# Optimization experiments

Hardware: AMD Instinct MI355X
Metric: run time of the kernel (lower is better)

Reference implementation:

```python
import jax, jax.numpy as jnp
import numpy as np

BS, TS, NE, ED = 32, 64, 64, 96
E = 256        # attn_embed_dim
H = 4          # attn_n_heads
HD = E // H    # head dim
RNN_H = 256
N_ACT = 32
NA = 16        # n_agents


def setup_inputs():
    key = jax.random.key(0)
    ks = jax.random.split(key, 40)
    entities = jax.random.normal(ks[0], (BS, TS, NE, ED), jnp.float32)
    obs_mask = jax.random.randint(ks[1], (BS, TS, NE, NE), 0, 2).astype(jnp.float32)  # 1 = masked
    entity_mask = (jax.random.uniform(ks[2], (BS, TS, NE)) < 0.1).astype(jnp.float32)  # 1 = inactive
    hidden_state = jnp.zeros((BS * NA, RNN_H), jnp.float32)
    it = iter(range(3, 40))
    def lin(fi, fo):
        return jax.random.normal(ks[next(it)], (fi, fo), jnp.float32) / np.sqrt(fi).astype(np.float32)
    p = dict(
        fc1_w=lin(ED, E), fc1_b=jnp.zeros((E,), jnp.float32),
        attn_in_w=lin(E, 3 * E), attn_out_w=lin(E, E), attn_out_b=jnp.zeros((E,), jnp.float32),
        fc2_w=lin(2 * E, RNN_H), fc2_b=jnp.zeros((RNN_H,), jnp.float32),
        gru_w_ih=lin(RNN_H, 3 * RNN_H), gru_w_hh=lin(RNN_H, 3 * RNN_H),
        gru_b_ih=jnp.zeros((3 * RNN_H,), jnp.float32), gru_b_hh=jnp.zeros((3 * RNN_H,), jnp.float32),
        fc3_w=lin(RNN_H, N_ACT), fc3_b=jnp.zeros((N_ACT,), jnp.float32),
        fcmsg1_w=lin(ED, E), fcmsg1_b=jnp.zeros((E,), jnp.float32),
        lmsg_in_w=lin(E, 3 * E), lmsg_out_w=lin(E, E), lmsg_out_b=jnp.zeros((E,), jnp.float32),
        gmsg_in_w=lin(E, 3 * E), gmsg_out_w=lin(E, E), gmsg_out_b=jnp.zeros((E,), jnp.float32),
        gate_in_w=lin(E, 3 * E), gate_out_w=lin(E, E), gate_out_b=jnp.zeros((E,), jnp.float32),
        gatefc1_w=lin(ED, E), gatefc1_b=jnp.zeros((E,), jnp.float32),
        gatefc2_w=lin(E, 2), gatefc2_b=jnp.zeros((2,), jnp.float32),
    )
    return dict(entities=entities, obs_mask=obs_mask, entity_mask=entity_mask,
                hidden_state=hidden_state, **p)


def _attn(x, in_w, out_w, out_b, pre_mask, post_mask):
    """REFIL EntityAttentionLayer: n_queries = NA agent rows, masks use 1 = masked."""
    B, ne, e = x.shape
    q, k, v = jnp.split(x @ in_w, 3, axis=-1)                       # each [B, ne, E]
    q = q[:, :NA].reshape(B, NA, H, HD).transpose(0, 2, 1, 3)        # [B, H, NA, HD]
    k = k.reshape(B, ne, H, HD).transpose(0, 2, 1, 3)                # [B, H, ne, HD]
    v = v.reshape(B, ne, H, HD).transpose(0, 2, 1, 3)
    logits = jnp.einsum('bhqd,bhkd->bhqk', q, k) / jnp.asarray(np.sqrt(HD), x.dtype)
    m = pre_mask[:, None, :NA, :]                                    # [B, 1, NA, ne]
    logits = jnp.where(m > 0, jnp.asarray(-1e9, x.dtype), logits)
    # softmax; zeroing masked cols also reproduces torch's NaN->0 for fully-masked rows
    w = jax.nn.softmax(logits, axis=-1) * (1.0 - m)
    out = jnp.einsum('bhqk,bhkd->bhqd', w, v).transpose(0, 2, 1, 3).reshape(B, NA, e)
    out = out @ out_w + out_b
    return out * (1.0 - post_mask[..., None])                        # masked_fill(post_mask, 0)


def _forward(entities, obs_mask, entity_mask, hidden_state,
             fc1_w, fc1_b, attn_in_w, attn_out_w, attn_out_b, fc2_w, fc2_b,
             gru_w_ih, gru_w_hh, gru_b_ih, gru_b_hh, fc3_w, fc3_b,
             fcmsg1_w, fcmsg1_b, lmsg_in_w, lmsg_out_w, lmsg_out_b,
             gmsg_in_w, gmsg_out_w, gmsg_out_b, gate_in_w, gate_out_w, gate_out_b,
             gatefc1_w, gatefc1_b, gatefc2_w, gatefc2_b):
    bs, ts, ne, ed = entities.shape
    B = bs * ts
    ent = entities.reshape(B, ne, ed)
    om = obs_mask.reshape(B, ne, ne)
    em = entity_mask.reshape(B, ne)
    agent_mask = em[:, :NA]                                          # [B, NA]
    full_obs_mask = 1.0 - (1.0 - agent_mask[:, None, :]) * (1.0 - agent_mask[:, :, None])

    x1 = jax.nn.relu(ent @ fc1_w + fc1_b)
    x2 = _attn(x1, attn_in_w, attn_out_w, attn_out_b, om, agent_mask)          # [B, NA, E]

    x1_msg = jax.nn.relu(ent @ fcmsg1_w + fcmsg1_b)
    x1_gate = jax.nn.relu(ent @ gatefc1_w + gatefc1_b)
    x2_msg = _attn(x1_msg, lmsg_in_w, lmsg_out_w, lmsg_out_b, om, agent_mask)  # [B, NA, E]
    x2_gate = _attn(x1_gate, gate_in_w, gate_out_w, gate_out_b, om, agent_mask)
    x2_gate = x2_gate @ gatefc2_w + gatefc2_b                                   # [B, NA, 2]

    # argmax of softmax == argmax of logits; gate in {0,1}, non-differentiable
    gate = jnp.argmax(x2_gate, axis=-1).astype(entities.dtype)
    gated_msg = x2_msg * gate[..., None]
    global_msg = _attn(gated_msg, gmsg_in_w, gmsg_out_w, gmsg_out_b,
                       full_obs_mask, agent_mask)                               # [B, NA, E]

    x3 = jax.nn.relu(jnp.concatenate([x2, global_msg], axis=-1) @ fc2_w + fc2_b)
    x3 = x3.reshape(bs, ts, NA, RNN_H)

    # GRU recurrence over ts via scan; hidden flattened to [bs*NA, RNN_H]
    h0 = hidden_state.reshape(-1, RNN_H)
    xs = x3.transpose(1, 0, 2, 3).reshape(ts, bs * NA, RNN_H)

    def step(h, x):
        gi = x @ gru_w_ih + gru_b_ih
        gh = h @ gru_w_hh + gru_b_hh
        ir, iz, inn = jnp.split(gi, 3, axis=-1)
        hr, hz, hn = jnp.split(gh, 3, axis=-1)
        r = jax.nn.sigmoid(ir + hr)
        z = jax.nn.sigmoid(iz + hz)
        n = jnp.tanh(inn + r * hn)
        h_new = (1.0 - z) * n + z * h
        return h_new, h_new

    _, hs = jax.lax.scan(step, h0, xs)                               # [ts, bs*NA, RNN_H]
    hs = hs.reshape(ts, bs, NA, RNN_H).transpose(1, 0, 2, 3)         # [bs, ts, NA, RNN_H]

    q = hs @ fc3_w + fc3_b                                           # [bs, ts, NA, N_ACT]
    am = agent_mask.reshape(bs, ts, NA, 1)
    q = q * (1.0 - am)                                               # masked_fill(agent_mask, 0)
    return q, hs, x2_gate


def reference(entities, obs_mask, entity_mask, hidden_state,
              fc1_w, fc1_b, attn_in_w, attn_out_w, attn_out_b, fc2_w, fc2_b,
              gru_w_ih, gru_w_hh, gru_b_ih, gru_b_hh, fc3_w, fc3_b,
              fcmsg1_w, fcmsg1_b, lmsg_in_w, lmsg_out_w, lmsg_out_b,
              gmsg_in_w, gmsg_out_w, gmsg_out_b, gate_in_w, gate_out_w, gate_out_b,
              gatefc1_w, gatefc1_b, gatefc2_w, gatefc2_b):
    return _forward(entities, obs_mask, entity_mask, hidden_state,
                    fc1_w, fc1_b, attn_in_w, attn_out_w, attn_out_b, fc2_w, fc2_b,
                    gru_w_ih, gru_w_hh, gru_b_ih, gru_b_hh, fc3_w, fc3_b,
                    fcmsg1_w, fcmsg1_b, lmsg_in_w, lmsg_out_w, lmsg_out_b,
                    gmsg_in_w, gmsg_out_w, gmsg_out_b, gate_in_w, gate_out_w, gate_out_b,
                    gatefc1_w, gatefc1_b, gatefc2_w, gatefc2_b)
```

## Files before the change

### kernel.cpp

```cpp
#include <hip/hip_runtime.h>


#define DEV __device__ __forceinline__

typedef _Float16 f16x8 __attribute__((ext_vector_type(8)));
typedef _Float16 f16x4 __attribute__((ext_vector_type(4)));
typedef float    f32x4 __attribute__((ext_vector_type(4)));
typedef float    f32x16 __attribute__((ext_vector_type(16)));

DEV f32x4 mfma16(f16x8 a, f16x8 b, f32x4 c){
  return __builtin_amdgcn_mfma_f32_16x16x32_f16(a, b, c, 0, 0, 0);
}
DEV f32x16 mfma32(f16x8 a, f16x8 b, f32x16 c){
  return __builtin_amdgcn_mfma_f32_32x32x16_f16(a, b, c, 0, 0, 0);
}

template<int MODE> struct AB {
  f16x8 hi, lo;
  DEV void mf(const AB& b, f32x4& c) const {
    if constexpr (MODE){
      c = mfma16(lo, b.hi, c);
      c = mfma16(hi, b.lo, c);
    }
    c = mfma16(hi, b.hi, c);
  }
};

template<int MODE> DEV AB<MODE> ldW(const _Float16* p, int losz){
  AB<MODE> r; r.hi = *(const f16x8*)p;
  if constexpr (MODE) r.lo = *(const f16x8*)(p + losz);
  return r;
}
template<int MODE> DEV AB<MODE> ldL(const _Float16* ph, const _Float16* pl){
  AB<MODE> r; r.hi = *(const f16x8*)ph;
  if constexpr (MODE) r.lo = *(const f16x8*)pl;
  return r;
}
template<int MODE> DEV AB<MODE> ldF(const float* p){
  AB<MODE> r;
  f32x4 v0 = *(const f32x4*)p, v1 = *(const f32x4*)(p + 4);
#pragma unroll
  for (int i = 0; i < 4; ++i){
    float a = v0[i], b = v1[i];
    _Float16 ah = (_Float16)a, bh = (_Float16)b;
    r.hi[i] = ah; r.hi[i+4] = bh;
    if constexpr (MODE){
      r.lo[i]   = (_Float16)(a - (float)ah);
      r.lo[i+4] = (_Float16)(b - (float)bh);
    }
  }
  return r;
}
template<int MODE> DEV void stL(_Float16* ph, _Float16* pl, int idx, float v){
  _Float16 h = (_Float16)v;
  ph[idx] = h;
  if constexpr (MODE) pl[idx] = (_Float16)(v - (float)h);
}

struct WJobs {
  const float* src[15];
  unsigned off[15];
  int K[15], N[15], mode[15];
};

__global__ __launch_bounds__(256) void k0_conv(WJobs jb, char* ws){
  const int job = blockIdx.y;
  const int K = jb.K[job], N = jb.N[job];
  const int total = K * N;
  _Float16* dh = (_Float16*)(ws + jb.off[job]);
  const float* src = jb.src[job];
  const int m = jb.mode[job];
  for (int idx = blockIdx.x*256 + threadIdx.x; idx < total; idx += gridDim.x*256){
    int n = idx / K, k = idx - n*K;
    float v = src[(size_t)k*N + n];
    _Float16 h = (_Float16)v;
    dh[idx] = h;
    if (m) dh[total + idx] = (_Float16)(v - (float)h);
  }
}

__global__ __launch_bounds__(256) void k0w_gate(
    const float* __restrict__ Wout, const float* __restrict__ Wg2,
    const float* __restrict__ bo,   const float* __restrict__ Win,
    _Float16* __restrict__ wveff, float* __restrict__ beff)
{
  __shared__ float weff_s[256*2];
  const int tid = threadIdx.x;
  {
    float a0 = 0.f, a1 = 0.f;
    const float* wr = Wout + (size_t)tid*256;
    for (int f = 0; f < 256; ++f){ float x = wr[f]; a0 += x*Wg2[2*f]; a1 += x*Wg2[2*f+1]; }
    weff_s[tid*2] = a0; weff_s[tid*2+1] = a1;
  }
  if (tid < 2){
    float s = 0.f;
    for (int f = 0; f < 256; ++f) s += bo[f]*Wg2[2*f + tid];
    beff[tid] = s;
  }
  __syncthreads();
  {
    const int j = tid;
    for (int n = 0; n < 16; ++n){
      float v = 0.f;
      if (n < 8){
        int h = n >> 1, c = n & 1;
        const float* wr = Win + (size_t)j*768 + 512 + h*64;
        const float* we = weff_s + (h*64)*2 + c;
        for (int d = 0; d < 64; ++d) v += wr[d]*we[2*d];
      }
      _Float16 hi = (_Float16)v;
      wveff[n*256 + j] = hi;
      wveff[16*256 + n*256 + j] = (_Float16)(v - (float)hi);
    }
  }
}

__global__ __launch_bounds__(512) void k1_all(
    const float* __restrict__ ent, const float* __restrict__ om, const float* __restrict__ em,
    const _Float16* __restrict__ W1a, const float* __restrict__ b1a,
    const _Float16* __restrict__ WINa,
    const _Float16* __restrict__ WOUTa, const float* __restrict__ boa,
    float* __restrict__ x2outa,
    const _Float16* __restrict__ W1b, const float* __restrict__ b1b,
    const _Float16* __restrict__ WINb,
    const _Float16* __restrict__ WOUTb, const float* __restrict__ bob,
    float* __restrict__ x2outb,
    const _Float16* __restrict__ W1g, const float* __restrict__ b1g,
    const _Float16* __restrict__ WINg,
    const _Float16* __restrict__ WVEFF,
    const float* __restrict__ beff, const float* __restrict__ gb2,
    float* __restrict__ og, float* __restrict__ gate)
{
  const int tid = threadIdx.x;
  const int w = tid >> 6, lg = (tid >> 4) & 3, li = tid & 15;
  extern __shared__ char smem[];

  if (blockIdx.x < 2048){
    const int br = blockIdx.x >> 10;
    const int p  = blockIdx.x & 1023;
    const int bb2[2] = { 2*p, 2*p + 1 };
    const _Float16* W1   = br ? W1b   : W1a;
    const float*    b1   = br ? b1b   : b1a;
    const _Float16* WIN  = br ? WINb  : WINa;
    const _Float16* WOUT = br ? WOUTb : WOUTa;
    const float*    bo   = br ? bob   : boa;
    float*          x2out= br ? x2outb: x2outa;

    const int wi = w & 3, ih = w >> 2;
    const int l = tid & 63;
    const int r32 = l & 31, kh = (l >> 5)*8;

    _Float16* x1   = (_Float16*)smem;
    _Float16* Ks   = (_Float16*)(smem + 67584);
    _Float16* Vs   = (_Float16*)(smem + 86016);
    _Float16* Qful = (_Float16*)(smem + 104448);
    float*    lgs  = (float*)(smem + 121344);
    _Float16* Ps   = (_Float16*)(smem + 130560);
    _Float16* outp = (_Float16*)(smem + 135168);

    {
      const int b = bb2[ih];
      _Float16* x1p = x1 + ih*16896;
      const int mt = wi & 1, ntb = (wi >> 1)*4;
      f32x16 acc0 = 0.f, acc1 = 0.f, acc2 = 0.f, acc3 = 0.f;
#pragma unroll
      for (int kk = 0; kk < 6; ++kk){
        AB<0> a = ldF<0>(ent + ((size_t)b*64 + mt*32 + r32)*96 + kk*16 + kh);
        f16x8 B0 = *(const f16x8*)(W1 + (size_t)((ntb + 0)*32 + r32)*96 + kk*16 + kh);
        f16x8 B1 = *(const f16x8*)(W1 + (size_t)((ntb + 1)*32 + r32)*96 + kk*16 + kh);
        f16x8 B2 = *(const f16x8*)(W1 + (size_t)((ntb + 2)*32 + r32)*96 + kk*16 + kh);
        f16x8 B3 = *(const f16x8*)(W1 + (size_t)((ntb + 3)*32 + r32)*96 + kk*16 + kh);
        acc0 = mfma32(a.hi, B0, acc0);
        acc1 = mfma32(a.hi, B1, acc1);
        acc2 = mfma32(a.hi, B2, acc2);
        acc3 = mfma32(a.hi, B3, acc3);
      }
#pragma unroll
      for (int s = 0; s < 4; ++s){
        const f32x16& ac = (s == 0) ? acc0 : (s == 1) ? acc1 : (s == 2) ? acc2 : acc3;
        int col = (ntb + s)*32 + r32;
        float bias = b1[col];
#pragma unroll
        for (int reg = 0; reg < 16; ++reg){
          int row = (reg & 3) + 8*(reg >> 2) + 4*(l >> 5);
          x1p[(mt*32 + row)*264 + col] = (_Float16)fmaxf(ac[reg] + bias, 0.f);
        }
      }
    }
    __syncthreads();

    {
      f32x16 acc = 0.f;
      const int itq = r32 >> 4, qr = r32 & 15;
      for (int kk = 0; kk < 16; ++kk){
        f16x8 A = *(const f16x8*)(x1 + itq*16896 + qr*264 + kk*16 + kh);
        f16x8 B = *(const f16x8*)(WIN + (size_t)(w*32 + r32)*256 + kk*16 + kh);
        acc = mfma32(A, B, acc);
      }
#pragma unroll
      for (int reg = 0; reg < 16; ++reg){
        int row = (reg & 3) + 8*(reg >> 2) + 4*(l >> 5);
        Qful[(row >> 4)*4224 + (row & 15)*264 + w*32 + r32] = (_Float16)acc[reg];
      }
    }
    __syncthreads();

    for (int h = 0; h < 4; ++h){
      if (w < 4){
        const int kt = w >> 1, dt = w & 1;
        f32x16 acc0 = 0.f, acc1 = 0.f;
        for (int kk = 0; kk < 16; ++kk){
          int ao = (kt*32 + r32)*264 + kk*16 + kh;
          f16x8 A0 = *(const f16x8*)(x1 + ao);
          f16x8 A1 = *(const f16x8*)(x1 + 16896 + ao);
          f16x8 B = *(const f16x8*)(WIN + (size_t)(256 + 64*h + dt*32 + r32)*256 + kk*16 + kh);
          acc0 = mfma32(A0, B, acc0);
          acc1 = mfma32(A1, B, acc1);
        }
#pragma unroll
        for (int reg = 0; reg < 16; ++reg){
          int row = (reg & 3) + 8*(reg >> 2) + 4*(l >> 5);
          Ks[(kt*32 + row)*72 + dt*32 + r32]        = (_Float16)acc0[reg];
          Ks[4608 + (kt*32 + row)*72 + dt*32 + r32] = (_Float16)acc1[reg];
        }
      } else {
        const int wv = w - 4;
        const int kt = wv >> 1, dt = wv & 1;
        f32x16 acc0 = 0.f, acc1 = 0.f;
        for (int kk = 0; kk < 16; ++kk){
          int ao = (kt*32 + r32)*264 + kk*16 + kh;
          f16x8 A0 = *(const f16x8*)(x1 + ao);
          f16x8 A1 = *(const f16x8*)(x1 + 16896 + ao);
          f16x8 B = *(const f16x8*)(WIN + (size_t)(512 + 64*h + dt*32 + r32)*256 + kk*16 + kh);
          acc0 = mfma32(A0, B, acc0);
          acc1 = mfma32(A1, B, acc1);
        }
#pragma unroll
        for (int rr = 0; rr < 4; ++rr){
          f16x4 p0, p1;
#pragma unroll
          for (int q4 = 0; q4 < 4; ++q4){
            p0[q4] = (_Float16)acc0[rr*4 + q4];
            p1[q4] = (_Float16)acc1[rr*4 + q4];
          }
          int key = kt*32 + rr*8 + 4*(l >> 5);
          *(f16x4*)(Vs + (dt*32 + r32)*72 + key)        = p0;
          *(f16x4*)(Vs + 4608 + (dt*32 + r32)*72 + key) = p1;
        }
      }
      __syncthreads();
      {
        const int b = bb2[ih];
        f32x4 acc = 0.f;
#pragma unroll
        for (int kk = 0; kk < 2; ++kk){
          f16x8 A = *(const f16x8*)(Qful + ih*4224 + li*264 + 64*h + kk*32 + lg*8);
          f16x8 B = *(const f16x8*)(Ks + ih*4608 + (16*wi + li)*72 + kk*32 + lg*8);
          acc = mfma16(A, B, acc);
        }
#pragma unroll
        for (int j = 0; j < 4; ++j){
          int q = 4*lg + j, key = 16*wi + li;
          float v = acc[j] * 0.125f;
          float m = om[((size_t)b*64 + q)*64 + key];
          if (m > 0.f) v = -1e9f;
          lgs[ih*1152 + q*72 + key] = v;
        }
      }
      __syncthreads();
      {
        const int it = tid >> 8, q = (tid >> 4) & 15, i16 = tid & 15;
        const int b = bb2[it];
        float pv[4], mx = -3e38f;
#pragma unroll
        for (int u = 0; u < 4; ++u){ pv[u] = lgs[it*1152 + q*72 + i16 + 16*u]; mx = fmaxf(mx, pv[u]); }
#pragma unroll
        for (int d = 1; d < 16; d <<= 1) mx = fmaxf(mx, __shfl_xor(mx, d, 16));
        float s = 0.f;
#pragma unroll
        for (int u = 0; u < 4; ++u){ pv[u] = expf(pv[u] - mx); s += pv[u]; }
#pragma unroll
        for (int d = 1; d < 16; d <<= 1) s += __shfl_xor(s, d, 16);
#pragma unroll
        for (int u = 0; u < 4; ++u){
          int key = i16 + 16*u;
          float m = om[((size_t)b*64 + q)*64 + key];
          Ps[it*1152 + q*72 + key] = (_Float16)((pv[u]/s)*(1.f - m));
        }
      }
      __syncthreads();
      {
        f32x4 acc = 0.f;
#pragma unroll
        for (int kk = 0; kk < 2; ++kk){
          f16x8 A = *(const f16x8*)(Ps + ih*1152 + li*72 + kk*32 + lg*8);
          f16x8 B = *(const f16x8*)(Vs + ih*4608 + (16*wi + li)*72 + kk*32 + lg*8);
          acc = mfma16(A, B, acc);
        }
#pragma unroll
        for (int j = 0; j < 4; ++j)
          outp[ih*4224 + (4*lg + j)*264 + 64*h + 16*wi + li] = (_Float16)acc[j];
      }
      __syncthreads();
    }

    {
      f32x16 acc = 0.f;
      const int ito = r32 >> 4, qr = r32 & 15;
      for (int kk = 0; kk < 16; ++kk){
        f16x8 A = *(const f16x8*)(outp + ito*4224 + qr*264 + kk*16 + kh);
        f16x8 B = *(const f16x8*)(WOUT + (size_t)(w*32 + r32)*256 + kk*16 + kh);
        acc = mfma32(A, B, acc);
      }
      int col = w*32 + r32;
      float bias = bo[col];
#pragma unroll
      for (int reg = 0; reg < 16; ++reg){
        int row = (reg & 3) + 8*(reg >> 2) + 4*(l >> 5);
        int it2 = row >> 4, q2 = row & 15;
        const int b = bb2[it2];
        float v = (acc[reg] + bias) * (1.f - em[(size_t)b*64 + q2]);
        x2out[((size_t)b*16 + q2)*256 + col] = v;
      }
    }
    return;
  }

  {
    constexpr int W1SZ = 96*256, WINSZ = 256*768, WVSZ = 16*256;
    const int b = blockIdx.x - 2048;
    const int l = tid & 63;
    const int r32 = l & 31, kh = (l >> 5)*8;

    char* sp = smem;
    _Float16* x1h = (_Float16*)sp; sp += 64*264*2;
    _Float16* x1l = (_Float16*)sp; sp += 64*264*2;
    _Float16* Kh  = (_Float16*)sp; sp += 64*72*2;
    _Float16* Kl  = (_Float16*)sp; sp += 64*72*2;
    _Float16* Qh  = (_Float16*)sp; sp += 16*264*2;
    _Float16* Ql  = (_Float16*)sp; sp += 16*264*2;
    float*    lgs = (float*)sp;    sp += 16*72*4;
    float*    Ps  = (float*)sp;    sp += 16*66*4;
    float*    v2s = (float*)sp;    sp += 64*18*4;
    float*  ogacc = (float*)sp;    sp += 32*4;
    float*  Kpart = (float*)sp;    sp += 8192*4;

    {
      const int mt = w & 1, ntb = (w >> 1)*2;
      f32x16 acc0 = 0.f, acc1 = 0.f;
#pragma unroll
      for (int kk = 0; kk < 6; ++kk){
        AB<1> a = ldF<1>(ent + ((size_t)b*64 + mt*32 + r32)*96 + kk*16 + kh);
#pragma unroll
        for (int s = 0; s < 2; ++s){
          const _Float16* bp = W1g + (size_t)((ntb + s)*32 + r32)*96 + kk*16 + kh;
          f16x8 Bh = *(const f16x8*)bp;
          f16x8 Bl = *(const f16x8*)(bp + W1SZ);
          f32x16& ac = s ? acc1 : acc0;
          ac = mfma32(a.lo, Bh, ac);
          ac = mfma32(a.hi, Bl, ac);
          ac = mfma32(a.hi, Bh, ac);
        }
      }
#pragma unroll
      for (int s = 0; s < 2; ++s){
        const f32x16& ac = s ? acc1 : acc0;
        int col = (ntb + s)*32 + r32;
        float bias = b1g[col];
#pragma unroll
        for (int reg = 0; reg < 16; ++reg){
          int row = (reg & 3) + 8*(reg >> 2) + 4*(l >> 5);
          stL<1>(x1h, x1l, (mt*32 + row)*264 + col, fmaxf(ac[reg] + bias, 0.f));
        }
      }
    }
    if (tid < 32) ogacc[tid] = 0.f;
    __syncthreads();

    {
#pragma unroll
      for (int s = 0; s < 2; ++s){
        int nt = w + s*8;
        f32x4 acc = 0.f;
        for (int kk = 0; kk < 8; ++kk){
          int ao = li*264 + kk*32 + lg*8;
          AB<1> a = ldL<1>(x1h + ao, x1l + ao);
          AB<1> bb = ldW<1>(WINg + (size_t)(nt*16 + li)*256 + kk*32 + lg*8, WINSZ);
          a.mf(bb, acc);
        }
#pragma unroll
        for (int j = 0; j < 4; ++j)
          stL<1>(Qh, Ql, (4*lg + j)*264 + nt*16 + li, acc[j]);
      }
      if (w < 4){
        f32x4 acc = 0.f;
        for (int kk = 0; kk < 8; ++kk){
          int ao = (w*16 + li)*264 + kk*32 + lg*8;
          AB<1> a = ldL<1>(x1h + ao, x1l + ao);
          AB<1> bb = ldW<1>(WVEFF + (size_t)li*256 + kk*32 + lg*8, WVSZ);
          a.mf(bb, acc);
        }
#pragma unroll
        for (int j = 0; j < 4; ++j)
          v2s[(w*16 + 4*lg + j)*18 + li] = acc[j];
      }
    }
    __syncthreads();

    for (int h = 0; h < 4; ++h){
      {
        const int t = w & 3, kt = t >> 1, dt = t & 1, khalf = w >> 2;
        f32x16 acc = 0.f;
#pragma unroll
        for (int k8 = 0; k8 < 8; ++k8){
          int ko = (khalf*8 + k8)*16 + kh;
          int ao = (kt*32 + r32)*264 + ko;
          f16x8 ah = *(const f16x8*)(x1h + ao);
          f16x8 al = *(const f16x8*)(x1l + ao);
          const _Float16* bp = WINg + (size_t)(256 + h*64 + dt*32 + r32)*256 + ko;
          f16x8 Bh = *(const f16x8*)bp;
          f16x8 Bl = *(const f16x8*)(bp + WINSZ);
          acc = mfma32(al, Bh, acc);
          acc = mfma32(ah, Bl, acc);
          acc = mfma32(ah, Bh, acc);
        }
#pragma unroll
        for (int reg = 0; reg < 16; ++reg){
          int row = (reg & 3) + 8*(reg >> 2) + 4*(l >> 5);
          Kpart[((khalf*4 + t)*32 + row)*32 + r32] = acc[reg];
        }
      }
      __syncthreads();
      {
        for (int e = tid; e < 4096; e += 512){
          float s2 = Kpart[e] + Kpart[4096 + e];
          int t2 = e >> 10, idx = e & 1023, row = idx >> 5, col = idx & 31;
          stL<1>(Kh, Kl, ((t2 >> 1)*32 + row)*72 + (t2 & 1)*32 + col, s2);
        }
      }
      __syncthreads();
      if (w < 4){
        f32x4 acc = 0.f;
#pragma unroll
        for (int kk = 0; kk < 2; ++kk){
          int ao = li*264 + h*64 + kk*32 + lg*8;
          AB<1> a = ldL<1>(Qh + ao, Ql + ao);
          int bo_ = (16*w + li)*72 + kk*32 + lg*8;
          AB<1> bb = ldL<1>(Kh + bo_, Kl + bo_);
          a.mf(bb, acc);
        }
#pragma unroll
        for (int j = 0; j < 4; ++j){
          int q = 4*lg + j, key = 16*w + li;
          float v = acc[j] * 0.125f;
          float m = om[((size_t)b*64 + q)*64 + key];
          if (m > 0.f) v = -1e9f;
          lgs[q*72 + key] = v;
        }
      }
      __syncthreads();
      if (tid < 256){
        int q = tid >> 4, i16 = tid & 15;
        float pv[4], mx = -3e38f;
#pragma unroll
        for (int u = 0; u < 4; ++u){ pv[u] = lgs[q*72 + i16 + 16*u]; mx = fmaxf(mx, pv[u]); }
#pragma unroll
        for (int d = 1; d < 16; d <<= 1) mx = fmaxf(mx, __shfl_xor(mx, d, 16));
        float s = 0.f;
#pragma unroll
        for (int u = 0; u < 4; ++u){ pv[u] = expf(pv[u] - mx); s += pv[u]; }
#pragma unroll
        for (int d = 1; d < 16; d <<= 1) s += __shfl_xor(s, d, 16);
#pragma unroll
        for (int u = 0; u < 4; ++u){
          int key = i16 + 16*u;
          float m = om[((size_t)b*64 + q)*64 + key];
          Ps[q*66 + key] = (pv[u]/s)*(1.f - m);
        }
      }
      __syncthreads();
      if (tid < 256){
        int q = tid >> 4, l16 = tid & 15;
        float a0 = 0.f, a1 = 0.f;
#pragma unroll
        for (int u = 0; u < 4; ++u){
          int k = l16 + 16*u;
          float p2 = Ps[q*66 + k];
          a0 += p2 * v2s[k*18 + h*2];
          a1 += p2 * v2s[k*18 + h*2 + 1];
        }
#pragma unroll
        for (int d = 1; d < 16; d <<= 1){ a0 += __shfl_xor(a0, d, 16); a1 += __shfl_xor(a1, d, 16); }
        if (l16 == 0){ ogacc[q*2] += a0; ogacc[q*2 + 1] += a1; }
      }
      __syncthreads();
    }
    if (tid < 16){
      int q = tid;
      float am = em[(size_t)b*64 + q];
      float g0 = (1.f - am)*(ogacc[2*q]     + beff[0]) + gb2[0];
      float g1 = (1.f - am)*(ogacc[2*q + 1] + beff[1]) + gb2[1];
      og[((size_t)b*16 + q)*2]     = g0;
      og[((size_t)b*16 + q)*2 + 1] = g1;
      gate[(size_t)b*16 + q] = (g1 > g0) ? 1.f : 0.f;
    }
  }
}

__global__ __launch_bounds__(256) void k2_global(
    const float* __restrict__ em,
    const float* __restrict__ x2, const float* __restrict__ x2m,
    const float* __restrict__ gate,
    const _Float16* __restrict__ GMIN, const _Float16* __restrict__ GMOUT, const float* __restrict__ gob,
    const _Float16* __restrict__ FC2T, const float* __restrict__ fc2b,
    const _Float16* __restrict__ GIHT, const float* __restrict__ gib,
    float* __restrict__ gi)
{
  const int p = blockIdx.x;
  const int tid = threadIdx.x;
  const int w = tid >> 6, lg = (tid >> 4) & 3, li = tid & 15;
  const int l = tid & 63;
  const int r32 = l & 31, kh = (l >> 5)*8;

  extern __shared__ char smem[];
  float*    gate_s = (float*)smem;
  _Float16* gm_s   = (_Float16*)(smem + 128);
  float*    lg2    = (float*)(smem + 17024);
  _Float16* P2     = (_Float16*)(smem + 20096);
  _Float16* outp   = (_Float16*)(smem + 22656);
  _Float16* x3_s   = (_Float16*)(smem + 39552);
  _Float16* Vtall  = (_Float16*)(smem + 56448);
  _Float16* Qall   = (_Float16*)(smem + 97408);
  _Float16* Kall   = (_Float16*)(smem + 114304);
  _Float16* cat_s  = (_Float16*)(smem + 97408);

  if (tid < 32){
    int it = tid >> 4, q = tid & 15;
    gate_s[it*16 + q] = gate[(size_t)(2*p + it)*16 + q];
  }
  __syncthreads();
#pragma unroll
  for (int it = 0; it < 2; ++it){
    const int b = 2*p + it;
    for (int idx = tid; idx < 4096; idx += 256){
      int q = idx >> 8, d = idx & 255;
      gm_s[it*4224 + q*264 + d] = (_Float16)(x2m[((size_t)b*16 + q)*256 + d] * gate_s[it*16 + q]);
    }
  }
  for (int idx = tid; idx < 10240; idx += 256) ((unsigned*)Vtall)[idx] = 0u;
  for (int idx = tid; idx < 2*16*40; idx += 256) P2[idx] = (_Float16)0.f;
  __syncthreads();

  {
    const int itq = r32 >> 4, qr = r32 & 15;
#pragma unroll
    for (int s = 0; s < 6; ++s){
      int nt = 6*w + s;
      f32x16 acc = 0.f;
      for (int kk = 0; kk < 16; ++kk){
        f16x8 A = *(const f16x8*)(gm_s + itq*4224 + qr*264 + kk*16 + kh);
        f16x8 B = *(const f16x8*)(GMIN + (size_t)(nt*32 + r32)*256 + kk*16 + kh);
        acc = mfma32(A, B, acc);
      }
      int sec = nt >> 3;
      int hcol = (nt & 7)*32 + r32;
#pragma unroll
      for (int reg = 0; reg < 16; ++reg){
        int row = (reg & 3) + 8*(reg >> 2) + 4*(l >> 5);
        int it2 = row >> 4, q2 = row & 15;
        _Float16 v = (_Float16)acc[reg];
        if (sec == 0)      Qall[it2*4224 + q2*264 + hcol] = v;
        else if (sec == 1) Kall[it2*4224 + q2*264 + hcol] = v;
        else               Vtall[it2*10240 + hcol*40 + q2] = v;
      }
    }
  }
  __syncthreads();

  for (int h = 0; h < 4; ++h){
    if (w < 2){
      const int it = w, b = 2*p + it;
      f32x4 acc = 0.f;
#pragma unroll
      for (int kk = 0; kk < 2; ++kk){
        f16x8 A = *(const f16x8*)(Qall + it*4224 + li*264 + 64*h + kk*32 + lg*8);
        f16x8 B = *(const f16x8*)(Kall + it*4224 + li*264 + 64*h + kk*32 + lg*8);
        acc = mfma16(A, B, acc);
      }
      float amk = em[(size_t)b*64 + li];
#pragma unroll
      for (int j = 0; j < 4; ++j){
        int q = 4*lg + j;
        float amq = em[(size_t)b*64 + q];
        float m = 1.f - (1.f - amq)*(1.f - amk);
        float v = acc[j]*0.125f;
        if (m > 0.f) v = -1e9f;
        lg2[it*384 + q*24 + li] = v;
      }
    }
    __syncthreads();
    {
      int q = tid >> 4, key = tid & 15;
#pragma unroll
      for (int it = 0; it < 2; ++it){
        const int b = 2*p + it;
        float v = lg2[it*384 + q*24 + key];
        float mx = v;
#pragma unroll
        for (int d = 1; d < 16; d <<= 1) mx = fmaxf(mx, __shfl_xor(mx, d, 16));
        float pe = expf(v - mx);
        float s = pe;
#pragma unroll
        for (int d = 1; d < 16; d <<= 1) s += __shfl_xor(s, d, 16);
        float amq = em[(size_t)b*64 + q], amk = em[(size_t)b*64 + key];
        float m = 1.f - (1.f - amq)*(1.f - amk);
        P2[it*640 + q*40 + key] = (_Float16)((pe/s)*(1.f - m));
      }
    }
    __syncthreads();
    {
#pragma unroll
      for (int it = 0; it < 2; ++it){
        f32x4 acc = 0.f;
        f16x8 A = *(const f16x8*)(P2 + it*640 + li*40 + lg*8);
        f16x8 B = *(const f16x8*)(Vtall + it*10240 + (size_t)(64*h + 16*w + li)*40 + lg*8);
        acc = mfma16(A, B, acc);
#pragma unroll
        for (int j = 0; j < 4; ++j)
          outp[it*4224 + (4*lg + j)*264 + 64*h + 16*w + li] = (_Float16)acc[j];
      }
    }
    __syncthreads();
  }
  {
    const int ito = r32 >> 4, qr = r32 & 15;
#pragma unroll
    for (int s = 0; s < 2; ++s){
      int nt = 2*w + s;
      f32x16 acc = 0.f;
      for (int kk = 0; kk < 16; ++kk){
        f16x8 A = *(const f16x8*)(outp + ito*4224 + qr*264 + kk*16 + kh);
        f16x8 B = *(const f16x8*)(GMOUT + (size_t)(nt*32 + r32)*256 + kk*16 + kh);
        acc = mfma32(A, B, acc);
      }
      int col = nt*32 + r32;
      float bias = gob[col];
#pragma unroll
      for (int reg = 0; reg < 16; ++reg){
        int row = (reg & 3) + 8*(reg >> 2) + 4*(l >> 5);
        int it2 = row >> 4, q2 = row & 15;
        float m = 1.f - em[(size_t)(2*p + it2)*64 + q2];
        cat_s[it2*8320 + q2*520 + 256 + col] = (_Float16)((acc[reg] + bias)*m);
      }
    }
#pragma unroll
    for (int it = 0; it < 2; ++it){
      const int b = 2*p + it;
      for (int idx = tid; idx < 4096; idx += 256){
        int q = idx >> 8, d = idx & 255;
        cat_s[it*8320 + q*520 + d] = (_Float16)(x2[((size_t)b*16 + q)*256 + d]);
      }
    }
  }
  __syncthreads();
  {
    const int ito = r32 >> 4, qr = r32 & 15;
#pragma unroll
    for (int s = 0; s < 2; ++s){
      int nt = 2*w + s;
      f32x16 acc = 0.f;
      for (int kk = 0; kk < 32; ++kk){
        f16x8 A = *(const f16x8*)(cat_s + ito*8320 + qr*520 + kk*16 + kh);
        f16x8 B = *(const f16x8*)(FC2T + (size_t)(nt*32 + r32)*512 + kk*16 + kh);
        acc = mfma32(A, B, acc);
      }
      int col = nt*32 + r32;
      float bias = fc2b[col];
#pragma unroll
      for (int reg = 0; reg < 16; ++reg){
        int row = (reg & 3) + 8*(reg >> 2) + 4*(l >> 5);
        int it2 = row >> 4, q2 = row & 15;
        x3_s[it2*4224 + q2*264 + col] = (_Float16)fmaxf(acc[reg] + bias, 0.f);
      }
    }
  }
  __syncthreads();
  {
    const int r0 = ((2*p) >> 6)*16, t0 = (2*p) & 63;
    const int ito = r32 >> 4, qr = r32 & 15;
#pragma unroll
    for (int s = 0; s < 6; ++s){
      int nt = 6*w + s;
      f32x16 acc = 0.f;
      for (int kk = 0; kk < 16; ++kk){
        f16x8 A = *(const f16x8*)(x3_s + ito*4224 + qr*264 + kk*16 + kh);
        f16x8 B = *(const f16x8*)(GIHT + (size_t)(nt*32 + r32)*256 + kk*16 + kh);
        acc = mfma32(A, B, acc);
      }
      int col = nt*32 + r32;
      float bias = gib[col];
#pragma unroll
      for (int reg = 0; reg < 16; ++reg){
        int row = (reg & 3) + 8*(reg >> 2) + 4*(l >> 5);
        int it2 = row >> 4, q2 = row & 15;
        gi[((size_t)((r0 + q2)*64 + t0 + it2))*768 + col] = acc[reg] + bias;
      }
    }
  }
}

__global__ __launch_bounds__(512) void k3_gru(
    const _Float16* __restrict__ WHH, const float* __restrict__ bhh,
    const float* __restrict__ gi, const float* __restrict__ h0,
    float* __restrict__ hs)
{
  const int rb = blockIdx.x;
  const int row0 = rb * 16;
  const int tid = threadIdx.x;
  const int w = tid >> 6, lg = (tid >> 4) & 3, li = tid & 15;

  extern __shared__ char smem3[];
  _Float16* hf16 = (_Float16*)smem3;
  float* hf32 = (float*)(smem3 + 8448);
  float* gh   = (float*)(smem3 + 8448 + 16640);
  float* bhs  = (float*)(smem3 + 8448 + 16640 + 49664);

  for (int idx = tid; idx < 768; idx += 512) bhs[idx] = bhh[idx];
  for (int idx = tid; idx < 4096; idx += 512){
    int r = idx >> 8, d = idx & 255;
    float v = h0[(size_t)(row0 + r)*256 + d];
    hf32[r*260 + d] = v;
    hf16[r*264 + d] = (_Float16)v;
  }
  __syncthreads();

  const int er = tid >> 5;
  const int dd = (tid & 31) * 8;

  for (int t = 0; t < 64; ++t){
    const float* gp = gi + ((size_t)(row0 + er)*64 + t)*768 + dd;
    f32x4 gr[2], gz[2], gn[2];
#pragma unroll
    for (int v = 0; v < 2; ++v){
      gr[v] = *(const f32x4*)(gp + v*4);
      gz[v] = *(const f32x4*)(gp + 256 + v*4);
      gn[v] = *(const f32x4*)(gp + 512 + v*4);
    }
    f16x8 a[8];
#pragma unroll
    for (int kk = 0; kk < 8; ++kk)
      a[kk] = *(const f16x8*)(hf16 + li*264 + kk*32 + lg*8);
    f32x4 acc[6];
#pragma unroll
    for (int c = 0; c < 6; ++c) acc[c] = 0.f;
#pragma unroll
    for (int c = 0; c < 6; ++c){
      const _Float16* bp = WHH + (size_t)(w*96 + c*16 + li)*256 + lg*8;
#pragma unroll
      for (int kk = 0; kk < 8; ++kk)
        acc[c] = mfma16(a[kk], *(const f16x8*)(bp + kk*32), acc[c]);
    }
#pragma unroll
    for (int c = 0; c < 6; ++c){
      int col = w*96 + c*16 + li;
#pragma unroll
      for (int j = 0; j < 4; ++j)
        gh[(4*lg + j)*776 + col] = acc[c][j];
    }
    __syncthreads();
    {
      float* hp32 = hf32 + er*260 + dd;
      float* hsp  = hs + ((size_t)(rb*64 + t)*16 + er)*256 + dd;
      f16x8 hv8;
#pragma unroll
      for (int v = 0; v < 2; ++v){
        f32x4 xr = *(const f32x4*)(gh + er*776 +       dd + v*4);
        f32x4 xz = *(const f32x4*)(gh + er*776 + 256 + dd + v*4);
        f32x4 xn = *(const f32x4*)(gh + er*776 + 512 + dd + v*4);
        f32x4 hold = *(const f32x4*)(hp32 + v*4);
        f32x4 hout;
#pragma unroll
        for (int e = 0; e < 4; ++e){
          int d = dd + v*4 + e;
          float rr_ = 1.f/(1.f + __expf(-(gr[v][e] + xr[e] + bhs[d])));
          float zz  = 1.f/(1.f + __expf(-(gz[v][e] + xz[e] + bhs[256 + d])));
          float pre = gn[v][e] + rr_*(xn[e] + bhs[512 + d]);
          float nn  = 1.f - 2.f/(1.f + __expf(2.f*pre));
          float hv = (1.f - zz)*nn + zz*hold[e];
          hout[e] = hv;
          hv8[v*4 + e] = (_Float16)hv;
        }
        *(f32x4*)(hp32 + v*4) = hout;
        *(f32x4*)(hsp + v*4)  = hout;
      }
      *(f16x8*)(hf16 + er*264 + dd) = hv8;
    }
    __syncthreads();
  }
}

__global__ __launch_bounds__(256) void k4_q(
    const _Float16* __restrict__ FC3T, const float* __restrict__ fc3b,
    const float* __restrict__ em, const float* __restrict__ hs, float* __restrict__ qo)
{
  const int tid = threadIdx.x;
  const int w = tid >> 6, lg = (tid >> 4) & 3, li = tid & 15;
  const int rb = blockIdx.x*64 + 16*w;
  f32x4 acc[2];
#pragma unroll
  for (int c = 0; c < 2; ++c) acc[c] = 0.f;
  for (int kk = 0; kk < 8; ++kk){
    const float* ap = hs + (size_t)(rb + li)*256 + kk*32 + lg*8;
    f32x4 v0 = *(const f32x4*)ap, v1 = *(const f32x4*)(ap + 4);
    f16x8 A;
#pragma unroll
    for (int e = 0; e < 4; ++e){ A[e] = (_Float16)v0[e]; A[e+4] = (_Float16)v1[e]; }
#pragma unroll
    for (int c = 0; c < 2; ++c){
      f16x8 B = *(const f16x8*)(FC3T + (size_t)(16*c + li)*256 + kk*32 + lg*8);
      acc[c] = mfma16(A, B, acc[c]);
    }
  }
#pragma unroll
  for (int c = 0; c < 2; ++c){
    int col = 16*c + li;
    float bias = fc3b[col];
#pragma unroll
    for (int j = 0; j < 4; ++j){
      int row = rb + 4*lg + j;
      float am = em[(size_t)(row >> 4)*64 + (row & 15)];
      qo[(size_t)row*32 + col] = (acc[c][j] + bias)*(1.f - am);
    }
  }
}

extern "C" void kernel_launch(void* const* d_in, const int* in_sizes, int n_in,
                              void* d_out, int out_size, void* d_ws, size_t ws_size,
                              hipStream_t stream)
{
  constexpr size_t OFF_FC1T   = 0;
  constexpr size_t OFF_MSG1T  = 49152;
  constexpr size_t OFF_AINT   = 98304;
  constexpr size_t OFF_LINT   = 491520;
  constexpr size_t OFF_AOUTT  = 884736;
  constexpr size_t OFF_LOUTT  = 1015808;
  constexpr size_t OFF_GMINT  = 1146880;
  constexpr size_t OFF_GMOUTT = 1540096;
  constexpr size_t OFF_FC2T   = 1671168;
  constexpr size_t OFF_GIHT   = 1933312;
  constexpr size_t OFF_GHHT   = 2326528;
  constexpr size_t OFF_FC3T   = 2719744;
  constexpr size_t OFF_G1T    = 2736128;
  constexpr size_t OFF_GINT   = 2834432;
  constexpr size_t OFF_WVEFF  = 3620864;
  constexpr size_t OFF_BEFF   = 3637248;
  constexpr size_t OFF_GATE   = 3637504;
  constexpr size_t OFF_X2     = 3768576;
  constexpr size_t OFF_X2M    = 37323008;
  constexpr size_t OFF_GI     = 70877440;
  constexpr size_t NEED       = 171540736;
  if (ws_size < NEED) return;

  char* ws = (char*)d_ws;
  const float* ent = (const float*)d_in[0];
  const float* om  = (const float*)d_in[1];
  const float* em  = (const float*)d_in[2];

  WJobs jb{};
  int nj = 0;
  auto addj = [&](int src_idx, size_t off, int K, int N, int m){
    jb.src[nj] = (const float*)d_in[src_idx]; jb.off[nj] = (unsigned)off;
    jb.K[nj] = K; jb.N[nj] = N; jb.mode[nj] = m; ++nj;
  };
  addj(4,  OFF_FC1T,   96, 256, 0);
  addj(17, OFF_MSG1T,  96, 256, 0);
  addj(6,  OFF_AINT,  256, 768, 0);
  addj(19, OFF_LINT,  256, 768, 0);
  addj(7,  OFF_AOUTT, 256, 256, 0);
  addj(20, OFF_LOUTT, 256, 256, 0);
  addj(22, OFF_GMINT, 256, 768, 0);
  addj(23, OFF_GMOUTT,256, 256, 0);
  addj(9,  OFF_FC2T,  512, 256, 0);
  addj(11, OFF_GIHT,  256, 768, 0);
  addj(12, OFF_GHHT,  256, 768, 0);
  addj(15, OFF_FC3T,  256,  32, 0);
  addj(28, OFF_G1T,    96, 256, 1);
  addj(25, OFF_GINT,  256, 768, 1);
  k0_conv<<<dim3(96, nj), 256, 0, stream>>>(jb, ws);

  k0w_gate<<<1, 256, 0, stream>>>(
      (const float*)d_in[26], (const float*)d_in[30],
      (const float*)d_in[27], (const float*)d_in[25],
      (_Float16*)(ws + OFF_WVEFF), (float*)(ws + OFF_BEFF));

  constexpr int SMB = 156672, SMK2 = 131200, SM3 = 77824;
  (void)hipFuncSetAttribute(reinterpret_cast<const void*>(&k1_all),
                            hipFuncAttributeMaxDynamicSharedMemorySize, SMB);
  (void)hipFuncSetAttribute(reinterpret_cast<const void*>(&k2_global),
                            hipFuncAttributeMaxDynamicSharedMemorySize, SMK2);
  (void)hipFuncSetAttribute(reinterpret_cast<const void*>(&k3_gru),
                            hipFuncAttributeMaxDynamicSharedMemorySize, SM3);

  float* qout = (float*)d_out;
  float* hsout = qout + 1048576;
  float* gout = qout + 9437184;

  k1_all<<<4096, 512, SMB, stream>>>(ent, om, em,
      (const _Float16*)(ws + OFF_FC1T),  (const float*)d_in[5],
      (const _Float16*)(ws + OFF_AINT),
      (const _Float16*)(ws + OFF_AOUTT), (const float*)d_in[8],
      (float*)(ws + OFF_X2),
      (const _Float16*)(ws + OFF_MSG1T), (const float*)d_in[18],
      (const _Float16*)(ws + OFF_LINT),
      (const _Float16*)(ws + OFF_LOUTT), (const float*)d_in[21],
      (float*)(ws + OFF_X2M),
      (const _Float16*)(ws + OFF_G1T),   (const float*)d_in[29],
      (const _Float16*)(ws + OFF_GINT),
      (const _Float16*)(ws + OFF_WVEFF),
      (const float*)(ws + OFF_BEFF), (const float*)d_in[31],
      gout, (float*)(ws + OFF_GATE));

  k2_global<<<1024, 256, SMK2, stream>>>(em,
      (const float*)(ws + OFF_X2), (const float*)(ws + OFF_X2M),
      (const float*)(ws + OFF_GATE),
      (const _Float16*)(ws + OFF_GMINT), (const _Float16*)(ws + OFF_GMOUTT), (const float*)d_in[24],
      (const _Float16*)(ws + OFF_FC2T), (const float*)d_in[10],
      (const _Float16*)(ws + OFF_GIHT), (const float*)d_in[13],
      (float*)(ws + OFF_GI));

  k3_gru<<<32, 512, SM3, stream>>>(
      (const _Float16*)(ws + OFF_GHHT), (const float*)d_in[14],
      (const float*)(ws + OFF_GI), (const float*)d_in[3], hsout);

  k4_q<<<512, 256, 0, stream>>>(
      (const _Float16*)(ws + OFF_FC3T), (const float*)d_in[16],
      em, hsout, qout);
}
```

Baseline: 1.144 ms.

## Split fused attention kernel into per-batch and gate kernels; widen GRU blocks

Splits the monolithic k1_all kernel into k1_b2, which handles one batch element per 512-thread block with about half the shared memory, and a separate k1_gate kernel for the high-precision gate branch. The aim is to raise occupancy and remove the mixed-branch dispatch inside one launch. The GRU recurrence kernel moves to 1024 threads, so each thread handles 4 columns instead of 8, which spreads the serial per-timestep work across more waves. The cost is an extra kernel launch, less reuse of weight loads across two batch elements, and more waves contending at each barrier in the GRU loop.

```diff
diff --git a/kernel.cpp b/kernel.cpp
--- a/kernel.cpp
+++ b/kernel.cpp
@@ -115,7 +115,7 @@
   }
 }
 
-__global__ __launch_bounds__(512) void k1_all(
+__global__ __launch_bounds__(512) void k1_b2(
     const float* __restrict__ ent, const float* __restrict__ om, const float* __restrict__ em,
     const _Float16* __restrict__ W1a, const float* __restrict__ b1a,
     const _Float16* __restrict__ WINa,
@@ -124,7 +124,183 @@
     const _Float16* __restrict__ W1b, const float* __restrict__ b1b,
     const _Float16* __restrict__ WINb,
     const _Float16* __restrict__ WOUTb, const float* __restrict__ bob,
-    float* __restrict__ x2outb,
+    float* __restrict__ x2outb)
+{
+  const int tid = threadIdx.x;
+  const int w = tid >> 6, lg = (tid >> 4) & 3, li = tid & 15;
+  const int l = tid & 63;
+  const int r32 = l & 31, kh = (l >> 5)*8;
+  extern __shared__ char smem[];
+
+  const int br = blockIdx.x >> 11;
+  const int b  = blockIdx.x & 2047;
+  const _Float16* W1   = br ? W1b   : W1a;
+  const float*    b1   = br ? b1b   : b1a;
+  const _Float16* WIN  = br ? WINb  : WINa;
+  const _Float16* WOUT = br ? WOUTb : WOUTa;
+  const float*    bo   = br ? bob   : boa;
+  float*          x2out= br ? x2outb: x2outa;
+
+  _Float16* x1   = (_Float16*)smem;
+  _Float16* Ks   = (_Float16*)(smem + 33792);
+  _Float16* Vs   = (_Float16*)(smem + 43008);
+  _Float16* Qful = (_Float16*)(smem + 52224);
+  float*    lgs  = (float*)(smem + 60672);
+  _Float16* Ps   = (_Float16*)(smem + 65280);
+  _Float16* outp = (_Float16*)(smem + 67584);
+
+  {
+    const int mt = w & 1, ntb = (w >> 1)*2;
+    f32x16 acc0 = 0.f, acc1 = 0.f;
+#pragma unroll
+    for (int kk = 0; kk < 6; ++kk){
+      AB<0> a = ldF<0>(ent + ((size_t)b*64 + mt*32 + r32)*96 + kk*16 + kh);
+      f16x8 B0 = *(const f16x8*)(W1 + (size_t)((ntb + 0)*32 + r32)*96 + kk*16 + kh);
+      f16x8 B1 = *(const f16x8*)(W1 + (size_t)((ntb + 1)*32 + r32)*96 + kk*16 + kh);
+      acc0 = mfma32(a.hi, B0, acc0);
+      acc1 = mfma32(a.hi, B1, acc1);
+    }
+#pragma unroll
+    for (int s = 0; s < 2; ++s){
+      const f32x16& ac = s ? acc1 : acc0;
+      int col = (ntb + s)*32 + r32;
+      float bias = b1[col];
+#pragma unroll
+      for (int reg = 0; reg < 16; ++reg){
+        int row = (reg & 3) + 8*(reg >> 2) + 4*(l >> 5);
+        x1[(mt*32 + row)*264 + col] = (_Float16)fmaxf(ac[reg] + bias, 0.f);
+      }
+    }
+  }
+  __syncthreads();
+
+  {
+#pragma unroll
+    for (int s = 0; s < 2; ++s){
+      int nt = w + s*8;
+      f32x4 acc = 0.f;
+      for (int kk = 0; kk < 8; ++kk){
+        f16x8 A = *(const f16x8*)(x1 + li*264 + kk*32 + lg*8);
+        f16x8 B = *(const f16x8*)(WIN + (size_t)(nt*16 + li)*256 + kk*32 + lg*8);
+        acc = mfma16(A, B, acc);
+      }
+#pragma unroll
+      for (int j = 0; j < 4; ++j)
+        Qful[(4*lg + j)*264 + nt*16 + li] = (_Float16)acc[j];
+    }
+  }
+  __syncthreads();
+
+  for (int h = 0; h < 4; ++h){
+    if (w < 4){
+      const int kt = w >> 1, dt = w & 1;
+      f32x16 acc = 0.f;
+      for (int kk = 0; kk < 16; ++kk){
+        f16x8 A = *(const f16x8*)(x1 + (kt*32 + r32)*264 + kk*16 + kh);
+        f16x8 B = *(const f16x8*)(WIN + (size_t)(256 + 64*h + dt*32 + r32)*256 + kk*16 + kh);
+        acc = mfma32(A, B, acc);
+      }
+#pragma unroll
+      for (int reg = 0; reg < 16; ++reg){
+        int row = (reg & 3) + 8*(reg >> 2) + 4*(l >> 5);
+        Ks[(kt*32 + row)*72 + dt*32 + r32] = (_Float16)acc[reg];
+      }
+    } else {
+      const int wv = w - 4;
+      const int kt = wv >> 1, dt = wv & 1;
+      f32x16 acc = 0.f;
+      for (int kk = 0; kk < 16; ++kk){
+        f16x8 A = *(const f16x8*)(x1 + (kt*32 + r32)*264 + kk*16 + kh);
+        f16x8 B = *(const f16x8*)(WIN + (size_t)(512 + 64*h + dt*32 + r32)*256 + kk*16 + kh);
+        acc = mfma32(A, B, acc);
+      }
+#pragma unroll
+      for (int rr = 0; rr < 4; ++rr){
+        f16x4 p0;
+#pragma unroll
+        for (int q4 = 0; q4 < 4; ++q4) p0[q4] = (_Float16)acc[rr*4 + q4];
+        int key = kt*32 + rr*8 + 4*(l >> 5);
+        *(f16x4*)(Vs + (dt*32 + r32)*72 + key) = p0;
+      }
+    }
+    __syncthreads();
+    if (w < 4){
+      f32x4 acc = 0.f;
+#pragma unroll
+      for (int kk = 0; kk < 2; ++kk){
+        f16x8 A = *(const f16x8*)(Qful + li*264 + 64*h + kk*32 + lg*8);
+        f16x8 B = *(const f16x8*)(Ks + (16*w + li)*72 + kk*32 + lg*8);
+        acc = mfma16(A, B, acc);
+      }
+#pragma unroll
+      for (int j = 0; j < 4; ++j){
+        int q = 4*lg + j, key = 16*w + li;
+        float v = acc[j] * 0.125f;
+        float m = om[((size_t)b*64 + q)*64 + key];
+        if (m > 0.f) v = -1e9f;
+        lgs[q*72 + key] = v;
+      }
+    }
+    __syncthreads();
+    if (tid < 256){
+      int q = tid >> 4, i16 = tid & 15;
+      float pv[4], mx = -3e38f;
+#pragma unroll
+      for (int u = 0; u < 4; ++u){ pv[u] = lgs[q*72 + i16 + 16*u]; mx = fmaxf(mx, pv[u]); }
+#pragma unroll
+      for (int d = 1; d < 16; d <<= 1) mx = fmaxf(mx, __shfl_xor(mx, d, 16));
+      float s = 0.f;
+#pragma unroll
+      for (int u = 0; u < 4; ++u){ pv[u] = expf(pv[u] - mx); s += pv[u]; }
+#pragma unroll
+      for (int d = 1; d < 16; d <<= 1) s += __shfl_xor(s, d, 16);
+#pragma unroll
+      for (int u = 0; u < 4; ++u){
+        int key = i16 + 16*u;
+        float m = om[((size_t)b*64 + q)*64 + key];
+        Ps[q*72 + key] = (_Float16)((pv[u]/s)*(1.f - m));
+      }
+    }
+    __syncthreads();
+    if (w < 4){
+      f32x4 acc = 0.f;
+#pragma unroll
+      for (int kk = 0; kk < 2; ++kk){
+        f16x8 A = *(const f16x8*)(Ps + li*72 + kk*32 + lg*8);
+        f16x8 B = *(const f16x8*)(Vs + (16*w + li)*72 + kk*32 + lg*8);
+        acc = mfma16(A, B, acc);
+      }
+#pragma unroll
+      for (int j = 0; j < 4; ++j)
+        outp[(4*lg + j)*264 + 64*h + 16*w + li] = (_Float16)acc[j];
+    }
+    __syncthreads();
+  }
+
+  {
+#pragma unroll
+    for (int s = 0; s < 2; ++s){
+      int nt = w + s*8;
+      f32x4 acc = 0.f;
+      for (int kk = 0; kk < 8; ++kk){
+        f16x8 A = *(const f16x8*)(outp + li*264 + kk*32 + lg*8);
+        f16x8 B = *(const f16x8*)(WOUT + (size_t)(nt*16 + li)*256 + kk*32 + lg*8);
+        acc = mfma16(A, B, acc);
+      }
+      int col = nt*16 + li;
+      float bias = bo[col];
+#pragma unroll
+      for (int j = 0; j < 4; ++j){
+        int q = 4*lg + j;
+        float v = (acc[j] + bias) * (1.f - em[(size_t)b*64 + q]);
+        x2out[((size_t)b*16 + q)*256 + col] = v;
+      }
+    }
+  }
+}
+
+__global__ __launch_bounds__(512) void k1_gate(
+    const float* __restrict__ ent, const float* __restrict__ om, const float* __restrict__ em,
     const _Float16* __restrict__ W1g, const float* __restrict__ b1g,
     const _Float16* __restrict__ WINg,
     const _Float16* __restrict__ WVEFF,
@@ -135,375 +311,182 @@
   const int w = tid >> 6, lg = (tid >> 4) & 3, li = tid & 15;
   extern __shared__ char smem[];
 
-  if (blockIdx.x < 2048){
-    const int br = blockIdx.x >> 10;
-    const int p  = blockIdx.x & 1023;
-    const int bb2[2] = { 2*p, 2*p + 1 };
-    const _Float16* W1   = br ? W1b   : W1a;
-    const float*    b1   = br ? b1b   : b1a;
-    const _Float16* WIN  = br ? WINb  : WINa;
-    const _Float16* WOUT = br ? WOUTb : WOUTa;
-    const float*    bo   = br ? bob   : boa;
-    float*          x2out= br ? x2outb: x2outa;
-
-    const int wi = w & 3, ih = w >> 2;
-    const int l = tid & 63;
-    const int r32 = l & 31, kh = (l >> 5)*8;
-
-    _Float16* x1   = (_Float16*)smem;
-    _Float16* Ks   = (_Float16*)(smem + 67584);
-    _Float16* Vs   = (_Float16*)(smem + 86016);
-    _Float16* Qful = (_Float16*)(smem + 104448);
-    float*    lgs  = (float*)(smem + 121344);
-    _Float16* Ps   = (_Float16*)(smem + 130560);
-    _Float16* outp = (_Float16*)(smem + 135168);
-
-    {
-      const int b = bb2[ih];
-      _Float16* x1p = x1 + ih*16896;
-      const int mt = wi & 1, ntb = (wi >> 1)*4;
-      f32x16 acc0 = 0.f, acc1 = 0.f, acc2 = 0.f, acc3 = 0.f;
-#pragma unroll
-      for (int kk = 0; kk < 6; ++kk){
-        AB<0> a = ldF<0>(ent + ((size_t)b*64 + mt*32 + r32)*96 + kk*16 + kh);
-        f16x8 B0 = *(const f16x8*)(W1 + (size_t)((ntb + 0)*32 + r32)*96 + kk*16 + kh);
-        f16x8 B1 = *(const f16x8*)(W1 + (size_t)((ntb + 1)*32 + r32)*96 + kk*16 + kh);
-        f16x8 B2 = *(const f16x8*)(W1 + (size_t)((ntb + 2)*32 + r32)*96 + kk*16 + kh);
-        f16x8 B3 = *(const f16x8*)(W1 + (size_t)((ntb + 3)*32 + r32)*96 + kk*16 + kh);
-        acc0 = mfma32(a.hi, B0, acc0);
-        acc1 = mfma32(a.hi, B1, acc1);
-        acc2 = mfma32(a.hi, B2, acc2);
-        acc3 = mfma32(a.hi, B3, acc3);
-      }
-#pragma unroll
-      for (int s = 0; s < 4; ++s){
-        const f32x16& ac = (s == 0) ? acc0 : (s == 1) ? acc1 : (s == 2) ? acc2 : acc3;
-        int col = (ntb + s)*32 + r32;
-        float bias = b1[col];
-#pragma unroll
-        for (int reg = 0; reg < 16; ++reg){
-          int row = (reg & 3) + 8*(reg >> 2) + 4*(l >> 5);
-          x1p[(mt*32 + row)*264 + col] = (_Float16)fmaxf(ac[reg] + bias, 0.f);
-        }
-      }
-    }
-    __syncthreads();
-
-    {
-      f32x16 acc = 0.f;
-      const int itq = r32 >> 4, qr = r32 & 15;
-      for (int kk = 0; kk < 16; ++kk){
-        f16x8 A = *(const f16x8*)(x1 + itq*16896 + qr*264 + kk*16 + kh);
-        f16x8 B = *(const f16x8*)(WIN + (size_t)(w*32 + r32)*256 + kk*16 + kh);
-        acc = mfma32(A, B, acc);
-      }
+  constexpr int W1SZ = 96*256, WINSZ = 256*768, WVSZ = 16*256;
+  const int b = blockIdx.x;
+  const int l = tid & 63;
+  const int r32 = l & 31, kh = (l >> 5)*8;
+
+  char* sp = smem;
+  _Float16* x1h = (_Float16*)sp; sp += 64*264*2;
+  _Float16* x1l = (_Float16*)sp; sp += 64*264*2;
+  _Float16* Kh  = (_Float16*)sp; sp += 64*72*2;
+  _Float16* Kl  = (_Float16*)sp; sp += 64*72*2;
+  _Float16* Qh  = (_Float16*)sp; sp += 16*264*2;
+  _Float16* Ql  = (_Float16*)sp; sp += 16*264*2;
+  float*    lgs = (float*)sp;    sp += 16*72*4;
+  float*    Ps  = (float*)sp;    sp += 16*66*4;
+  float*    v2s = (float*)sp;    sp += 64*18*4;
+  float*  ogacc = (float*)sp;    sp += 32*4;
+  float*  Kpart = (float*)sp;    sp += 8192*4;
+
+  {
+    const int mt = w & 1, ntb = (w >> 1)*2;
+    f32x16 acc0 = 0.f, acc1 = 0.f;
+#pragma unroll
+    for (int kk = 0; kk < 6; ++kk){
+      AB<1> a = ldF<1>(ent + ((size_t)b*64 + mt*32 + r32)*96 + kk*16 + kh);
+#pragma unroll
+      for (int s = 0; s < 2; ++s){
+        const _Float16* bp = W1g + (size_t)((ntb + s)*32 + r32)*96 + kk*16 + kh;
+        f16x8 Bh = *(const f16x8*)bp;
+        f16x8 Bl = *(const f16x8*)(bp + W1SZ);
+        f32x16& ac = s ? acc1 : acc0;
+        ac = mfma32(a.lo, Bh, ac);
+        ac = mfma32(a.hi, Bl, ac);
+        ac = mfma32(a.hi, Bh, ac);
+      }
+    }
+#pragma unroll
+    for (int s = 0; s < 2; ++s){
+      const f32x16& ac = s ? acc1 : acc0;
+      int col = (ntb + s)*32 + r32;
+      float bias = b1g[col];
 #pragma unroll
       for (int reg = 0; reg < 16; ++reg){
         int row = (reg & 3) + 8*(reg >> 2) + 4*(l >> 5);
-        Qful[(row >> 4)*4224 + (row & 15)*264 + w*32 + r32] = (_Float16)acc[reg];
-      }
-    }
-    __syncthreads();
-
-    for (int h = 0; h < 4; ++h){
-      if (w < 4){
-        const int kt = w >> 1, dt = w & 1;
-        f32x16 acc0 = 0.f, acc1 = 0.f;
-        for (int kk = 0; kk < 16; ++kk){
-          int ao = (kt*32 + r32)*264 + kk*16 + kh;
-          f16x8 A0 = *(const f16x8*)(x1 + ao);
-          f16x8 A1 = *(const f16x8*)(x1 + 16896 + ao);
-          f16x8 B = *(const f16x8*)(WIN + (size_t)(256 + 64*h + dt*32 + r32)*256 + kk*16 + kh);
-          acc0 = mfma32(A0, B, acc0);
-          acc1 = mfma32(A1, B, acc1);
-        }
-#pragma unroll
-        for (int reg = 0; reg < 16; ++reg){
-          int row = (reg & 3) + 8*(reg >> 2) + 4*(l >> 5);
-          Ks[(kt*32 + row)*72 + dt*32 + r32]        = (_Float16)acc0[reg];
-          Ks[4608 + (kt*32 + row)*72 + dt*32 + r32] = (_Float16)acc1[reg];
-        }
-      } else {
-        const int wv = w - 4;
-        const int kt = wv >> 1, dt = wv & 1;
-        f32x16 acc0 = 0.f, acc1 = 0.f;
-        for (int kk = 0; kk < 16; ++kk){
-          int ao = (kt*32 + r32)*264 + kk*16 + kh;
-          f16x8 A0 = *(const f16x8*)(x1 + ao);
-          f16x8 A1 = *(const f16x8*)(x1 + 16896 + ao);
-          f16x8 B = *(const f16x8*)(WIN + (size_t)(512 + 64*h + dt*32 + r32)*256 + kk*16 + kh);
-          acc0 = mfma32(A0, B, acc0);
-          acc1 = mfma32(A1, B, acc1);
-        }
-#pragma unroll
-        for (int rr = 0; rr < 4; ++rr){
-          f16x4 p0, p1;
-#pragma unroll
-          for (int q4 = 0; q4 < 4; ++q4){
-            p0[q4] = (_Float16)acc0[rr*4 + q4];
-            p1[q4] = (_Float16)acc1[rr*4 + q4];
-          }
-          int key = kt*32 + rr*8 + 4*(l >> 5);
-          *(f16x4*)(Vs + (dt*32 + r32)*72 + key)        = p0;
-          *(f16x4*)(Vs + 4608 + (dt*32 + r32)*72 + key) = p1;
-        }
-      }
-      __syncthreads();
-      {
-        const int b = bb2[ih];
-        f32x4 acc = 0.f;
-#pragma unroll
-        for (int kk = 0; kk < 2; ++kk){
-          f16x8 A = *(const f16x8*)(Qful + ih*4224 + li*264 + 64*h + kk*32 + lg*8);
-          f16x8 B = *(const f16x8*)(Ks + ih*4608 + (16*wi + li)*72 + kk*32 + lg*8);
-          acc = mfma16(A, B, acc);
-        }
-#pragma unroll
-        for (int j = 0; j < 4; ++j){
-          int q = 4*lg + j, key = 16*wi + li;
-          float v = acc[j] * 0.125f;
-          float m = om[((size_t)b*64 + q)*64 + key];
-          if (m > 0.f) v = -1e9f;
-          lgs[ih*1152 + q*72 + key] = v;
-        }
-      }
-      __syncthreads();
-      {
-        const int it = tid >> 8, q = (tid >> 4) & 15, i16 = tid & 15;
-        const int b = bb2[it];
-        float pv[4], mx = -3e38f;
-#pragma unroll
-        for (int u = 0; u < 4; ++u){ pv[u] = lgs[it*1152 + q*72 + i16 + 16*u]; mx = fmaxf(mx, pv[u]); }
-#pragma unroll
-        for (int d = 1; d < 16; d <<= 1) mx = fmaxf(mx, __shfl_xor(mx, d, 16));
-        float s = 0.f;
-#pragma unroll
-        for (int u = 0; u < 4; ++u){ pv[u] = expf(pv[u] - mx); s += pv[u]; }
-#pragma unroll
-        for (int d = 1; d < 16; d <<= 1) s += __shfl_xor(s, d, 16);
-#pragma unroll
-        for (int u = 0; u < 4; ++u){
-          int key = i16 + 16*u;
-          float m = om[((size_t)b*64 + q)*64 + key];
-          Ps[it*1152 + q*72 + key] = (_Float16)((pv[u]/s)*(1.f - m));
-        }
-      }
-      __syncthreads();
-      {
-        f32x4 acc = 0.f;
-#pragma unroll
-        for (int kk = 0; kk < 2; ++kk){
-          f16x8 A = *(const f16x8*)(Ps + ih*1152 + li*72 + kk*32 + lg*8);
-          f16x8 B = *(const f16x8*)(Vs + ih*4608 + (16*wi + li)*72 + kk*32 + lg*8);
-          acc = mfma16(A, B, acc);
-        }
-#pragma unroll
-        for (int j = 0; j < 4; ++j)
-          outp[ih*4224 + (4*lg + j)*264 + 64*h + 16*wi + li] = (_Float16)acc[j];
-      }
-      __syncthreads();
-    }
-
+        stL<1>(x1h, x1l, (mt*32 + row)*264 + col, fmaxf(ac[reg] + bias, 0.f));
+      }
+    }
+  }
+  if (tid < 32) ogacc[tid] = 0.f;
+  __syncthreads();
+
+  {
+#pragma unroll
+    for (int s = 0; s < 2; ++s){
+      int nt = w + s*8;
+      f32x4 acc = 0.f;
+      for (int kk = 0; kk < 8; ++kk){
+        int ao = li*264 + kk*32 + lg*8;
+        AB<1> a = ldL<1>(x1h + ao, x1l + ao);
+        AB<1> bb = ldW<1>(WINg + (size_t)(nt*16 + li)*256 + kk*32 + lg*8, WINSZ);
+        a.mf(bb, acc);
+      }
+#pragma unroll
+      for (int j = 0; j < 4; ++j)
+        stL<1>(Qh, Ql, (4*lg + j)*264 + nt*16 + li, acc[j]);
+    }
+    if (w < 4){
+      f32x4 acc = 0.f;
+      for (int kk = 0; kk < 8; ++kk){
+        int ao = (w*16 + li)*264 + kk*32 + lg*8;
+        AB<1> a = ldL<1>(x1h + ao, x1l + ao);
+        AB<1> bb = ldW<1>(WVEFF + (size_t)li*256 + kk*32 + lg*8, WVSZ);
+        a.mf(bb, acc);
+      }
+#pragma unroll
+      for (int j = 0; j < 4; ++j)
+        v2s[(w*16 + 4*lg + j)*18 + li] = acc[j];
+    }
+  }
+  __syncthreads();
+
+  for (int h = 0; h < 4; ++h){
     {
+      const int t = w & 3, kt = t >> 1, dt = t & 1, khalf = w >> 2;
       f32x16 acc = 0.f;
-      const int ito = r32 >> 4, qr = r32 & 15;
-      for (int kk = 0; kk < 16; ++kk){
-        f16x8 A = *(const f16x8*)(outp + ito*4224 + qr*264 + kk*16 + kh);
-        f16x8 B = *(const f16x8*)(WOUT + (size_t)(w*32 + r32)*256 + kk*16 + kh);
-        acc = mfma32(A, B, acc);
-      }
-      int col = w*32 + r32;
-      float bias = bo[col];
+#pragma unroll
+      for (int k8 = 0; k8 < 8; ++k8){
+        int ko = (khalf*8 + k8)*16 + kh;
+        int ao = (kt*32 + r32)*264 + ko;
+        f16x8 ah = *(const f16x8*)(x1h + ao);
+        f16x8 al = *(const f16x8*)(x1l + ao);
+        const _Float16* bp = WINg + (size_t)(256 + h*64 + dt*32 + r32)*256 + ko;
+        f16x8 Bh = *(const f16x8*)bp;
+        f16x8 Bl = *(const f16x8*)(bp + WINSZ);
+        acc = mfma32(al, Bh, acc);
+        acc = mfma32(ah, Bl, acc);
+        acc = mfma32(ah, Bh, acc);
+      }
 #pragma unroll
       for (int reg = 0; reg < 16; ++reg){
         int row = (reg & 3) + 8*(reg >> 2) + 4*(l >> 5);
-        int it2 = row >> 4, q2 = row & 15;
-        const int b = bb2[it2];
-        float v = (acc[reg] + bias) * (1.f - em[(size_t)b*64 + q2]);
-        x2out[((size_t)b*16 + q2)*256 + col] = v;
-      }
-    }
-    return;
-  }
-
-  {
-    constexpr int W1SZ = 96*256, WINSZ = 256*768, WVSZ = 16*256;
-    const int b = blockIdx.x - 2048;
-    const int l = tid & 63;
-    const int r32 = l & 31, kh = (l >> 5)*8;
-
-    char* sp = smem;
-    _Float16* x1h = (_Float16*)sp; sp += 64*264*2;
-    _Float16* x1l = (_Float16*)sp; sp += 64*264*2;
-    _Float16* Kh  = (_Float16*)sp; sp += 64*72*2;
-    _Float16* Kl  = (_Float16*)sp; sp += 64*72*2;
-    _Float16* Qh  = (_Float16*)sp; sp += 16*264*2;
-    _Float16* Ql  = (_Float16*)sp; sp += 16*264*2;
-    float*    lgs = (float*)sp;    sp += 16*72*4;
-    float*    Ps  = (float*)sp;    sp += 16*66*4;
-    float*    v2s = (float*)sp;    sp += 64*18*4;
-    float*  ogacc = (float*)sp;    sp += 32*4;
-    float*  Kpart = (float*)sp;    sp += 8192*4;
-
+        Kpart[((khalf*4 + t)*32 + row)*32 + r32] = acc[reg];
+      }
+    }
+    __syncthreads();
     {
-      const int mt = w & 1, ntb = (w >> 1)*2;
-      f32x16 acc0 = 0.f, acc1 = 0.f;
-#pragma unroll
-      for (int kk = 0; kk < 6; ++kk){
-        AB<1> a = ldF<1>(ent + ((size_t)b*64 + mt*32 + r32)*96 + kk*16 + kh);
-#pragma unroll
-        for (int s = 0; s < 2; ++s){
-          const _Float16* bp = W1g + (size_t)((ntb + s)*32 + r32)*96 + kk*16 + kh;
-          f16x8 Bh = *(const f16x8*)bp;
-          f16x8 Bl = *(const f16x8*)(bp + W1SZ);
-          f32x16& ac = s ? acc1 : acc0;
-          ac = mfma32(a.lo, Bh, ac);
-          ac = mfma32(a.hi, Bl, ac);
-          ac = mfma32(a.hi, Bh, ac);
-        }
-      }
-#pragma unroll
-      for (int s = 0; s < 2; ++s){
-        const f32x16& ac = s ? acc1 : acc0;
-        int col = (ntb + s)*32 + r32;
-        float bias = b1g[col];
-#pragma unroll
-        for (int reg = 0; reg < 16; ++reg){
-          int row = (reg & 3) + 8*(reg >> 2) + 4*(l >> 5);
-          stL<1>(x1h, x1l, (mt*32 + row)*264 + col, fmaxf(ac[reg] + bias, 0.f));
-        }
-      }
-    }
-    if (tid < 32) ogacc[tid] = 0.f;
-    __syncthreads();
-
-    {
-#pragma unroll
-      for (int s = 0; s < 2; ++s){
-        int nt = w + s*8;
-        f32x4 acc = 0.f;
-        for (int kk = 0; kk < 8; ++kk){
-          int ao = li*264 + kk*32 + lg*8;
-          AB<1> a = ldL<1>(x1h + ao, x1l + ao);
-          AB<1> bb = ldW<1>(WINg + (size_t)(nt*16 + li)*256 + kk*32 + lg*8, WINSZ);
-          a.mf(bb, acc);
-        }
-#pragma unroll
-        for (int j = 0; j < 4; ++j)
-          stL<1>(Qh, Ql, (4*lg + j)*264 + nt*16 + li, acc[j]);
-      }
-      if (w < 4){
-        f32x4 acc = 0.f;
-        for (int kk = 0; kk < 8; ++kk){
-          int ao = (w*16 + li)*264 + kk*32 + lg*8;
-          AB<1> a = ldL<1>(x1h + ao, x1l + ao);
-          AB<1> bb = ldW<1>(WVEFF + (size_t)li*256 + kk*32 + lg*8, WVSZ);
-          a.mf(bb, acc);
-        }
-#pragma unroll
-        for (int j = 0; j < 4; ++j)
-          v2s[(w*16 + 4*lg + j)*18 + li] = acc[j];
-      }
-    }
-    __syncthreads();
-
-    for (int h = 0; h < 4; ++h){
-      {
-        const int t = w & 3, kt = t >> 1, dt = t & 1, khalf = w >> 2;
-        f32x16 acc = 0.f;
-#pragma unroll
-        for (int k8 = 0; k8 < 8; ++k8){
-          int ko = (khalf*8 + k8)*16 + kh;
-          int ao = (kt*32 + r32)*264 + ko;
-          f16x8 ah = *(const f16x8*)(x1h + ao);
-          f16x8 al = *(const f16x8*)(x1l + ao);
-          const _Float16* bp = WINg + (size_t)(256 + h*64 + dt*32 + r32)*256 + ko;
-          f16x8 Bh = *(const f16x8*)bp;
-          f16x8 Bl = *(const f16x8*)(bp + WINSZ);
-          acc = mfma32(al, Bh, acc);
-          acc = mfma32(ah, Bl, acc);
-          acc = mfma32(ah, Bh, acc);
-        }
-#pragma unroll
-        for (int reg = 0; reg < 16; ++reg){
-          int row = (reg & 3) + 8*(reg >> 2) + 4*(l >> 5);
-          Kpart[((khalf*4 + t)*32 + row)*32 + r32] = acc[reg];
-        }
-      }
-      __syncthreads();
-      {
-        for (int e = tid; e < 4096; e += 512){
-          float s2 = Kpart[e] + Kpart[4096 + e];
-          int t2 = e >> 10, idx = e & 1023, row = idx >> 5, col = idx & 31;
-          stL<1>(Kh, Kl, ((t2 >> 1)*32 + row)*72 + (t2 & 1)*32 + col, s2);
-        }
-      }
-      __syncthreads();
-      if (w < 4){
-        f32x4 acc = 0.f;
-#pragma unroll
-        for (int kk = 0; kk < 2; ++kk){
-          int ao = li*264 + h*64 + kk*32 + lg*8;
-          AB<1> a = ldL<1>(Qh + ao, Ql + ao);
-          int bo_ = (16*w + li)*72 + kk*32 + lg*8;
-          AB<1> bb = ldL<1>(Kh + bo_, Kl + bo_);
-          a.mf(bb, acc);
-        }
-#pragma unroll
-        for (int j = 0; j < 4; ++j){
-          int q = 4*lg + j, key = 16*w + li;
-          float v = acc[j] * 0.125f;
-          float m = om[((size_t)b*64 + q)*64 + key];
-          if (m > 0.f) v = -1e9f;
-          lgs[q*72 + key] = v;
-        }
-      }
-      __syncthreads();
-      if (tid < 256){
-        int q = tid >> 4, i16 = tid & 15;
-        float pv[4], mx = -3e38f;
-#pragma unroll
-        for (int u = 0; u < 4; ++u){ pv[u] = lgs[q*72 + i16 + 16*u]; mx = fmaxf(mx, pv[u]); }
-#pragma unroll
-        for (int d = 1; d < 16; d <<= 1) mx = fmaxf(mx, __shfl_xor(mx, d, 16));
-        float s = 0.f;
-#pragma unroll
-        for (int u = 0; u < 4; ++u){ pv[u] = expf(pv[u] - mx); s += pv[u]; }
-#pragma unroll
-        for (int d = 1; d < 16; d <<= 1) s += __shfl_xor(s, d, 16);
-#pragma unroll
-        for (int u = 0; u < 4; ++u){
-          int key = i16 + 16*u;
-          float m = om[((size_t)b*64 + q)*64 + key];
-          Ps[q*66 + key] = (pv[u]/s)*(1.f - m);
-        }
-      }
-      __syncthreads();
-      if (tid < 256){
-        int q = tid >> 4, l16 = tid & 15;
-        float a0 = 0.f, a1 = 0.f;
-#pragma unroll
-        for (int u = 0; u < 4; ++u){
-          int k = l16 + 16*u;
-          float p2 = Ps[q*66 + k];
-          a0 += p2 * v2s[k*18 + h*2];
-          a1 += p2 * v2s[k*18 + h*2 + 1];
-        }
-#pragma unroll
-        for (int d = 1; d < 16; d <<= 1){ a0 += __shfl_xor(a0, d, 16); a1 += __shfl_xor(a1, d, 16); }
-        if (l16 == 0){ ogacc[q*2] += a0; ogacc[q*2 + 1] += a1; }
-      }
-      __syncthreads();
-    }
-    if (tid < 16){
-      int q = tid;
-      float am = em[(size_t)b*64 + q];
-      float g0 = (1.f - am)*(ogacc[2*q]     + beff[0]) + gb2[0];
-      float g1 = (1.f - am)*(ogacc[2*q + 1] + beff[1]) + gb2[1];
-      og[((size_t)b*16 + q)*2]     = g0;
-      og[((size_t)b*16 + q)*2 + 1] = g1;
-      gate[(size_t)b*16 + q] = (g1 > g0) ? 1.f : 0.f;
-    }
+      for (int e = tid; e < 4096; e += 512){
+        float s2 = Kpart[e] + Kpart[4096 + e];
+        int t2 = e >> 10, idx = e & 1023, row = idx >> 5, col = idx & 31;
+        stL<1>(Kh, Kl, ((t2 >> 1)*32 + row)*72 + (t2 & 1)*32 + col, s2);
+      }
+    }
+    __syncthreads();
+    if (w < 4){
+      f32x4 acc = 0.f;
+#pragma unroll
+      for (int kk = 0; kk < 2; ++kk){
+        int ao = li*264 + h*64 + kk*32 + lg*8;
+        AB<1> a = ldL<1>(Qh + ao, Ql + ao);
+        int bo_ = (16*w + li)*72 + kk*32 + lg*8;
+        AB<1> bb = ldL<1>(Kh + bo_, Kl + bo_);
+        a.mf(bb, acc);
+      }
+#pragma unroll
+      for (int j = 0; j < 4; ++j){
+        int q = 4*lg + j, key = 16*w + li;
+        float v = acc[j] * 0.125f;
+        float m = om[((size_t)b*64 + q)*64 + key];
+        if (m > 0.f) v = -1e9f;
+        lgs[q*72 + key] = v;
+      }
+    }
+    __syncthreads();
+    if (tid < 256){
+      int q = tid >> 4, i16 = tid & 15;
+      float pv[4], mx = -3e38f;
+#pragma unroll
+      for (int u = 0; u < 4; ++u){ pv[u] = lgs[q*72 + i16 + 16*u]; mx = fmaxf(mx, pv[u]); }
+#pragma unroll
+      for (int d = 1; d < 16; d <<= 1) mx = fmaxf(mx, __shfl_xor(mx, d, 16));
+      float s = 0.f;
+#pragma unroll
+      for (int u = 0; u < 4; ++u){ pv[u] = expf(pv[u] - mx); s += pv[u]; }
+#pragma unroll
+      for (int d = 1; d < 16; d <<= 1) s += __shfl_xor(s, d, 16);
+#pragma unroll
+      for (int u = 0; u < 4; ++u){
+        int key = i16 + 16*u;
+        float m = om[((size_t)b*64 + q)*64 + key];
+        Ps[q*66 + key] = (pv[u]/s)*(1.f - m);
+      }
+    }
+    __syncthreads();
+    if (tid < 256){
+      int q = tid >> 4, l16 = tid & 15;
+      float a0 = 0.f, a1 = 0.f;
+#pragma unroll
+      for (int u = 0; u < 4; ++u){
+        int k = l16 + 16*u;
+        float p2 = Ps[q*66 + k];
+        a0 += p2 * v2s[k*18 + h*2];
+        a1 += p2 * v2s[k*18 + h*2 + 1];
+      }
+#pragma unroll
+      for (int d = 1; d < 16; d <<= 1){ a0 += __shfl_xor(a0, d, 16); a1 += __shfl_xor(a1, d, 16); }
+      if (l16 == 0){ ogacc[q*2] += a0; ogacc[q*2 + 1] += a1; }
+    }
+    __syncthreads();
+  }
+  if (tid < 16){
+    int q = tid;
+    float am = em[(size_t)b*64 + q];
+    float g0 = (1.f - am)*(ogacc[2*q]     + beff[0]) + gb2[0];
+    float g1 = (1.f - am)*(ogacc[2*q + 1] + beff[1]) + gb2[1];
+    og[((size_t)b*16 + q)*2]     = g0;
+    og[((size_t)b*16 + q)*2 + 1] = g1;
+    gate[(size_t)b*16 + q] = (g1 > g0) ? 1.f : 0.f;
   }
 }
 
@@ -709,7 +692,7 @@
   }
 }
 
-__global__ __launch_bounds__(512) void k3_gru(
+__global__ __launch_bounds__(1024) void k3_gru(
     const _Float16* __restrict__ WHH, const float* __restrict__ bhh,
     const float* __restrict__ gi, const float* __restrict__ h0,
     float* __restrict__ hs)
@@ -725,8 +708,8 @@
   float* gh   = (float*)(smem3 + 8448 + 16640);
   float* bhs  = (float*)(smem3 + 8448 + 16640 + 49664);
 
-  for (int idx = tid; idx < 768; idx += 512) bhs[idx] = bhh[idx];
-  for (int idx = tid; idx < 4096; idx += 512){
+  for (int idx = tid; idx < 768; idx += 1024) bhs[idx] = bhh[idx];
+  for (int idx = tid; idx < 4096; idx += 1024){
     int r = idx >> 8, d = idx & 255;
     float v = h0[(size_t)(row0 + r)*256 + d];
     hf32[r*260 + d] = v;
@@ -734,35 +717,31 @@
   }
   __syncthreads();
 
-  const int er = tid >> 5;
-  const int dd = (tid & 31) * 8;
+  const int er = tid >> 6;
+  const int dd = (tid & 63) * 4;
 
   for (int t = 0; t < 64; ++t){
     const float* gp = gi + ((size_t)(row0 + er)*64 + t)*768 + dd;
-    f32x4 gr[2], gz[2], gn[2];
-#pragma unroll
-    for (int v = 0; v < 2; ++v){
-      gr[v] = *(const f32x4*)(gp + v*4);
-      gz[v] = *(const f32x4*)(gp + 256 + v*4);
-      gn[v] = *(const f32x4*)(gp + 512 + v*4);
-    }
+    f32x4 gr = *(const f32x4*)(gp);
+    f32x4 gz = *(const f32x4*)(gp + 256);
+    f32x4 gn = *(const f32x4*)(gp + 512);
     f16x8 a[8];
 #pragma unroll
     for (int kk = 0; kk < 8; ++kk)
       a[kk] = *(const f16x8*)(hf16 + li*264 + kk*32 + lg*8);
-    f32x4 acc[6];
-#pragma unroll
-    for (int c = 0; c < 6; ++c) acc[c] = 0.f;
-#pragma unroll
-    for (int c = 0; c < 6; ++c){
-      const _Float16* bp = WHH + (size_t)(w*96 + c*16 + li)*256 + lg*8;
+    f32x4 acc[3];
+#pragma unroll
+    for (int c = 0; c < 3; ++c) acc[c] = 0.f;
+#pragma unroll
+    for (int c = 0; c < 3; ++c){
+      const _Float16* bp = WHH + (size_t)(w*48 + c*16 + li)*256 + lg*8;
 #pragma unroll
       for (int kk = 0; kk < 8; ++kk)
         acc[c] = mfma16(a[kk], *(const f16x8*)(bp + kk*32), acc[c]);
     }
 #pragma unroll
-    for (int c = 0; c < 6; ++c){
-      int col = w*96 + c*16 + li;
+    for (int c = 0; c < 3; ++c){
+      int col = w*48 + c*16 + li;
 #pragma unroll
       for (int j = 0; j < 4; ++j)
         gh[(4*lg + j)*776 + col] = acc[c][j];
@@ -771,29 +750,26 @@
     {
       float* hp32 = hf32 + er*260 + dd;
       float* hsp  = hs + ((size_t)(rb*64 + t)*16 + er)*256 + dd;
-      f16x8 hv8;
-#pragma unroll
-      for (int v = 0; v < 2; ++v){
-        f32x4 xr = *(const f32x4*)(gh + er*776 +       dd + v*4);
-        f32x4 xz = *(const f32x4*)(gh + er*776 + 256 + dd + v*4);
-        f32x4 xn = *(const f32x4*)(gh + er*776 + 512 + dd + v*4);
-        f32x4 hold = *(const f32x4*)(hp32 + v*4);
-        f32x4 hout;
-#pragma unroll
-        for (int e = 0; e < 4; ++e){
-          int d = dd + v*4 + e;
-          float rr_ = 1.f/(1.f + __expf(-(gr[v][e] + xr[e] + bhs[d])));
-          float zz  = 1.f/(1.f + __expf(-(gz[v][e] + xz[e] + bhs[256 + d])));
-          float pre = gn[v][e] + rr_*(xn[e] + bhs[512 + d]);
-          float nn  = 1.f - 2.f/(1.f + __expf(2.f*pre));
-          float hv = (1.f - zz)*nn + zz*hold[e];
-          hout[e] = hv;
-          hv8[v*4 + e] = (_Float16)hv;
-        }
-        *(f32x4*)(hp32 + v*4) = hout;
-        *(f32x4*)(hsp + v*4)  = hout;
-      }
-      *(f16x8*)(hf16 + er*264 + dd) = hv8;
+      f32x4 xr = *(const f32x4*)(gh + er*776 +       dd);
+      f32x4 xz = *(const f32x4*)(gh + er*776 + 256 + dd);
+      f32x4 xn = *(const f32x4*)(gh + er*776 + 512 + dd);
+      f32x4 hold = *(const f32x4*)(hp32);
+      f32x4 hout;
+      f16x4 hv4;
+#pragma unroll
+      for (int e = 0; e < 4; ++e){
+        int d = dd + e;
+        float rr_ = 1.f/(1.f + __expf(-(gr[e] + xr[e] + bhs[d])));
+        float zz  = 1.f/(1.f + __expf(-(gz[e] + xz[e] + bhs[256 + d])));
+        float pre = gn[e] + rr_*(xn[e] + bhs[512 + d]);
+        float nn  = 1.f - 2.f/(1.f + __expf(2.f*pre));
+        float hv = (1.f - zz)*nn + zz*hold[e];
+        hout[e] = hv;
+        hv4[e] = (_Float16)hv;
+      }
+      *(f32x4*)(hp32) = hout;
+      *(f32x4*)(hsp)  = hout;
+      *(f16x4*)(hf16 + er*264 + dd) = hv4;
     }
     __syncthreads();
   }
@@ -893,9 +869,11 @@
       (const float*)d_in[27], (const float*)d_in[25],
       (_Float16*)(ws + OFF_WVEFF), (float*)(ws + OFF_BEFF));
 
-  constexpr int SMB = 156672, SMK2 = 131200, SM3 = 77824;
-  (void)hipFuncSetAttribute(reinterpret_cast<const void*>(&k1_all),
-                            hipFuncAttributeMaxDynamicSharedMemorySize, SMB);
+  constexpr int SMB2 = 76032, SMG = 149248, SMK2 = 131200, SM3 = 77824;
+  (void)hipFuncSetAttribute(reinterpret_cast<const void*>(&k1_b2),
+                            hipFuncAttributeMaxDynamicSharedMemorySize, SMB2);
+  (void)hipFuncSetAttribute(reinterpret_cast<const void*>(&k1_gate),
+                            hipFuncAttributeMaxDynamicSharedMemorySize, SMG);
   (void)hipFuncSetAttribute(reinterpret_cast<const void*>(&k2_global),
                             hipFuncAttributeMaxDynamicSharedMemorySize, SMK2);
   (void)hipFuncSetAttribute(reinterpret_cast<const void*>(&k3_gru),
@@ -905,7 +883,7 @@
   float* hsout = qout + 1048576;
   float* gout = qout + 9437184;
 
-  k1_all<<<4096, 512, SMB, stream>>>(ent, om, em,
+  k1_b2<<<4096, 512, SMB2, stream>>>(ent, om, em,
       (const _Float16*)(ws + OFF_FC1T),  (const float*)d_in[5],
       (const _Float16*)(ws + OFF_AINT),
       (const _Float16*)(ws + OFF_AOUTT), (const float*)d_in[8],
@@ -913,7 +891,9 @@
       (const _Float16*)(ws + OFF_MSG1T), (const float*)d_in[18],
       (const _Float16*)(ws + OFF_LINT),
       (const _Float16*)(ws + OFF_LOUTT), (const float*)d_in[21],
-      (float*)(ws + OFF_X2M),
+      (float*)(ws + OFF_X2M));
+
+  k1_gate<<<2048, 512, SMG, stream>>>(ent, om, em,
       (const _Float16*)(ws + OFF_G1T),   (const float*)d_in[29],
       (const _Float16*)(ws + OFF_GINT),
       (const _Float16*)(ws + OFF_WVEFF),
@@ -928,7 +908,7 @@
       (const _Float16*)(ws + OFF_GIHT), (const float*)d_in[13],
       (float*)(ws + OFF_GI));
 
-  k3_gru<<<32, 512, SM3, stream>>>(
+  k3_gru<<<32, 1024, SM3, stream>>>(
       (const _Float16*)(ws + OFF_GHHT), (const float*)d_in[14],
       (const float*)(ws + OFF_GI), (const float*)d_in[3], hsout);
 
```

Result: slower. 1.297 ms (+13.4%).
